# Kernel tuning notes

Measured on AMD Instinct MI355X. Metric: run time of the kernel, lower is better.

Reference implementation:

```python
import jax, jax.numpy as jnp
import numpy as np


def setup_inputs() -> dict:
    key = jax.random.key(0)
    k1, k2, k3 = jax.random.split(key, 3)
    B, S, I, H, M = 8, 2048, 256, 256, 1024
    x = jax.random.normal(k1, (B, S, I), dtype=jnp.float32)
    mem = jax.random.normal(k2, (B, M, H), dtype=jnp.float32)
    # Xavier-uniform with gain=sqrt(2): bound = sqrt(2)*sqrt(6/(H+I))
    bound = np.sqrt(2.0) * np.sqrt(6.0 / (H + I))
    W = jax.random.uniform(k3, (H, I), dtype=jnp.float32, minval=-bound, maxval=bound)
    return {"x": x, "mem": mem, "W": W}


def reference(x, mem, W):
    # key[b,s,h] = relu(sum_i x[b,s,i] * W[h,i])  -- one batched GEMM for all t
    key_seq = jax.nn.relu(jnp.einsum("bsi,hi->bsh", x, W))
    # val[b,s,m] = sum_h key[b,s,h] * mem[b,m,h]
    val_seq = jnp.einsum("bsh,bmh->bsm", key_seq, mem)
    return key_seq, val_seq
```

## Files before the change

kernel.cpp:

```cpp
#include <hip/hip_runtime.h>
#include <cstdint>

typedef unsigned short u16;
typedef __bf16 bf16x8 __attribute__((ext_vector_type(8)));
typedef float f32x4 __attribute__((ext_vector_type(4)));
typedef u16 u16x8 __attribute__((ext_vector_type(8)));

#define NX 4194304L
#define NW 65536L
#define NM 2097152L
#define WS_MEM (NW)
#define WS_KEY (NW + NM)

__device__ __forceinline__ u16 f2bf_rne(float f) {
  union { float f; uint32_t u; } v; v.f = f;
  uint32_t r = v.u + 0x7fffu + ((v.u >> 16) & 1u);
  return (u16)(r >> 16);
}

__global__ void convert_bf16_kernel(const float* __restrict__ mem,
                                    const float* __restrict__ W,
                                    u16* __restrict__ ws) {
  long e = ((long)blockIdx.x * blockDim.x + threadIdx.x) * 8;
  if (e >= NW + NM) return;
  const float* src; long l;
  if (e < NW) { src = W;   l = e; }
  else        { src = mem; l = e - NW; }
  float4 f0 = *(const float4*)(src + l);
  float4 f1 = *(const float4*)(src + l + 4);
  u16x8 o;
  o[0]=f2bf_rne(f0.x); o[1]=f2bf_rne(f0.y); o[2]=f2bf_rne(f0.z); o[3]=f2bf_rne(f0.w);
  o[4]=f2bf_rne(f1.x); o[5]=f2bf_rne(f1.y); o[6]=f2bf_rne(f1.z); o[7]=f2bf_rne(f1.w);
  *(u16x8*)(ws + e) = o;
}

#define BM 128
#define BN 128
#define BK 32

__device__ __forceinline__ u16x8 cvt8(float4 a, float4 b) {
  u16x8 o;
  o[0]=f2bf_rne(a.x); o[1]=f2bf_rne(a.y); o[2]=f2bf_rne(a.z); o[3]=f2bf_rne(a.w);
  o[4]=f2bf_rne(b.x); o[5]=f2bf_rne(b.y); o[6]=f2bf_rne(b.z); o[7]=f2bf_rne(b.w);
  return o;
}

template<bool CONVERT_A, bool RELU, bool STORE_BF16>
__global__ __launch_bounds__(256, 3)
void gemm_nt(const void* __restrict__ Ap, const u16* __restrict__ B,
             float* __restrict__ C, u16* __restrict__ Cbf,
             int M, int N, int K,
             long sA_batch, long sB_batch, long sC_batch)
{
  __shared__ __align__(16) u16 sA[2][BM * BK];
  __shared__ __align__(16) u16 sB[2][BN * BK];
  const int tid  = threadIdx.x;
  const int wave = tid >> 6;
  const int lane = tid & 63;
  const int quad = lane >> 4;
  const int r    = lane & 15;
  const int wm   = wave >> 1;
  const int wn   = wave & 1;

  const int gx  = gridDim.x, gy = gridDim.y;
  const int nwg = gx * gy * (int)gridDim.z;
  const int id  = (int)blockIdx.x + gx * ((int)blockIdx.y + gy * (int)blockIdx.z);
  const int cpx = nwg >> 3;
  const int lid = (id & 7) * cpx + (id >> 3);
  const int bx  = lid % gx;
  const int tq  = lid / gx;
  const int by  = tq % gy;
  const int bz  = tq / gy;

  const int bm   = by * BM;
  const int bn   = bx * BN;
  const int batch = bz;

  const float* Af = CONVERT_A ? ((const float*)Ap + (long)batch * sA_batch) : nullptr;
  const char*  Ab = CONVERT_A ? nullptr : (const char*)((const u16*)Ap + (long)batch * sA_batch);
  const char*  Bb = (const char*)(B + (long)batch * sB_batch);
  const long ldr = (long)K * 2;

  f32x4 acc[4][4];
  #pragma unroll
  for (int i = 0; i < 4; i++)
    #pragma unroll
    for (int j = 0; j < 4; j++)
      acc[i][j] = f32x4{0.f, 0.f, 0.f, 0.f};

  const int o0 = wave * 1024 + lane * 16;

  auto stageB = [&](int buf, int kt) {
    #pragma unroll
    for (int rr = 0; rr < 2; rr++) {
      const int o    = rr * 4096 + o0;
      const int row  = o >> 6;
      const int colb = o & 63;
      const char* g = Bb + (long)(bn + row) * ldr + (long)kt * 2 + colb;
      char* l = (char*)&sB[buf][0] + rr * 4096 + wave * 1024;
      __builtin_amdgcn_global_load_lds((const __attribute__((address_space(1))) void*)g,
                                       (__attribute__((address_space(3))) void*)l, 16, 0, 0);
    }
  };
  auto stageA_lds = [&](int buf, int kt) {
    #pragma unroll
    for (int rr = 0; rr < 2; rr++) {
      const int o    = rr * 4096 + o0;
      const int row  = o >> 6;
      const int colb = o & 63;
      const char* g = Ab + (long)(bm + row) * ldr + (long)kt * 2 + colb;
      char* l = (char*)&sA[buf][0] + rr * 4096 + wave * 1024;
      __builtin_amdgcn_global_load_lds((const __attribute__((address_space(1))) void*)g,
                                       (__attribute__((address_space(3))) void*)l, 16, 0, 0);
    }
  };

  float4 xa[4];
  const int arow = tid >> 1;
  const int ac0  = (tid & 1) * 16;
  auto loadA_f32 = [&](int kt) {
    const float* g = Af + (long)(bm + arow) * K + kt + ac0;
    #pragma unroll
    for (int c = 0; c < 4; c++) xa[c] = *(const float4*)(g + c * 4);
  };
  auto writeA_cvt = [&](int buf) {
    u16* d = &sA[buf][arow * BK + ac0];
    *(u16x8*)d       = cvt8(xa[0], xa[1]);
    *(u16x8*)(d + 8) = cvt8(xa[2], xa[3]);
  };

  if (CONVERT_A) { loadA_f32(0); writeA_cvt(0); }
  else           { stageA_lds(0, 0); }
  stageB(0, 0);
  __syncthreads();

  const int NT = K / BK;
  for (int t = 0; t < NT; ++t) {
    const int cur = t & 1, nxt = cur ^ 1;
    const bool pf = (t + 1 < NT);
    if (pf) {
      if (CONVERT_A) loadA_f32((t + 1) * BK);
      else           stageA_lds(nxt, (t + 1) * BK);
      stageB(nxt, (t + 1) * BK);
    }

    bf16x8 af[4], bfr[4];
    #pragma unroll
    for (int i = 0; i < 4; i++)
      af[i] = *(const bf16x8*)&sA[cur][(wm * 64 + i * 16 + r) * BK + quad * 8];
    #pragma unroll
    for (int j = 0; j < 4; j++)
      bfr[j] = *(const bf16x8*)&sB[cur][(wn * 64 + j * 16 + r) * BK + quad * 8];
    #pragma unroll
    for (int i = 0; i < 4; i++)
      #pragma unroll
      for (int j = 0; j < 4; j++)
        acc[i][j] = __builtin_amdgcn_mfma_f32_16x16x32_bf16(af[i], bfr[j], acc[i][j], 0, 0, 0);

    if (CONVERT_A && pf) writeA_cvt(nxt);
    __syncthreads();
  }

  float* Co = C + (long)batch * sC_batch;
  u16*   Bo = STORE_BF16 ? (Cbf + (long)batch * sC_batch) : nullptr;
  #pragma unroll
  for (int i = 0; i < 4; i++) {
    #pragma unroll
    for (int j = 0; j < 4; j++) {
      #pragma unroll
      for (int reg = 0; reg < 4; reg++) {
        const int row = bm + wm * 64 + i * 16 + quad * 4 + reg;
        const int col = bn + wn * 64 + j * 16 + r;
        float v = acc[i][j][reg];
        if (RELU) v = v > 0.f ? v : 0.f;
        const long idx = (long)row * N + col;
        Co[idx] = v;
        if (STORE_BF16) Bo[idx] = f2bf_rne(v);
      }
    }
  }
}

extern "C" void kernel_launch(void* const* d_in, const int* in_sizes, int n_in,
                              void* d_out, int out_size, void* d_ws, size_t ws_size,
                              hipStream_t stream) {
  const float* x   = (const float*)d_in[0];
  const float* mem = (const float*)d_in[1];
  const float* W   = (const float*)d_in[2];
  float* out   = (float*)d_out;
  float* key_f = out;
  float* val_f = out + NX;
  u16* ws     = (u16*)d_ws;
  u16* W_bf   = ws;
  u16* mem_bf = ws + WS_MEM;
  u16* key_bf = ws + WS_KEY;

  convert_bf16_kernel<<<(int)((NW + NM) / 8 / 256), 256, 0, stream>>>(mem, W, ws);

  dim3 g1(256 / BN, 16384 / BM, 1);
  gemm_nt<true, true, true><<<g1, 256, 0, stream>>>(x, W_bf, key_f, key_bf,
                                                    16384, 256, 256, 0, 0, 0);

  dim3 g2(1024 / BN, 2048 / BM, 8);
  gemm_nt<false, false, false><<<g2, 256, 0, stream>>>(key_bf, mem_bf, val_f, nullptr,
                                                       2048, 1024, 256,
                                                       (long)2048 * 256, (long)1024 * 256,
                                                       (long)2048 * 1024);
}
```

Before: 126.0 us.

## Fuse bf16 conversion into GEMM loads and drop separate convert kernel

Removes the standalone fp32-to-bf16 conversion kernel and the bf16 key copy. Both GEMMs now read fp32 operands directly and convert them in registers before writing to LDS. This saves one launch plus the workspace writes and reads. In exchange, B operands are read as fp32 (twice the bytes, re-read by many tiles), and the async global_load_lds path is replaced by register-staged loads with conversion ALU work.

```diff
diff --git a/kernel.cpp b/kernel.cpp
--- a/kernel.cpp
+++ b/kernel.cpp
@@ -7,36 +7,12 @@
 typedef u16 u16x8 __attribute__((ext_vector_type(8)));
 
 #define NX 4194304L
-#define NW 65536L
-#define NM 2097152L
-#define WS_MEM (NW)
-#define WS_KEY (NW + NM)
 
 __device__ __forceinline__ u16 f2bf_rne(float f) {
   union { float f; uint32_t u; } v; v.f = f;
   uint32_t r = v.u + 0x7fffu + ((v.u >> 16) & 1u);
   return (u16)(r >> 16);
 }
-
-__global__ void convert_bf16_kernel(const float* __restrict__ mem,
-                                    const float* __restrict__ W,
-                                    u16* __restrict__ ws) {
-  long e = ((long)blockIdx.x * blockDim.x + threadIdx.x) * 8;
-  if (e >= NW + NM) return;
-  const float* src; long l;
-  if (e < NW) { src = W;   l = e; }
-  else        { src = mem; l = e - NW; }
-  float4 f0 = *(const float4*)(src + l);
-  float4 f1 = *(const float4*)(src + l + 4);
-  u16x8 o;
-  o[0]=f2bf_rne(f0.x); o[1]=f2bf_rne(f0.y); o[2]=f2bf_rne(f0.z); o[3]=f2bf_rne(f0.w);
-  o[4]=f2bf_rne(f1.x); o[5]=f2bf_rne(f1.y); o[6]=f2bf_rne(f1.z); o[7]=f2bf_rne(f1.w);
-  *(u16x8*)(ws + e) = o;
-}
-
-#define BM 128
-#define BN 128
-#define BK 32
 
 __device__ __forceinline__ u16x8 cvt8(float4 a, float4 b) {
   u16x8 o;
@@ -45,12 +21,16 @@
   return o;
 }
 
-template<bool CONVERT_A, bool RELU, bool STORE_BF16>
+#define BM 128
+#define BN 128
+#define BK 32
+
+template<bool RELU>
 __global__ __launch_bounds__(256, 3)
-void gemm_nt(const void* __restrict__ Ap, const u16* __restrict__ B,
-             float* __restrict__ C, u16* __restrict__ Cbf,
-             int M, int N, int K,
-             long sA_batch, long sB_batch, long sC_batch)
+void gemm_nt_f32(const float* __restrict__ A, const float* __restrict__ B,
+                 float* __restrict__ C,
+                 int M, int N, int K,
+                 long sA_batch, long sB_batch, long sC_batch)
 {
   __shared__ __align__(16) u16 sA[2][BM * BK];
   __shared__ __align__(16) u16 sB[2][BN * BK];
@@ -72,14 +52,12 @@
   const int by  = tq % gy;
   const int bz  = tq / gy;
 
-  const int bm   = by * BM;
-  const int bn   = bx * BN;
+  const int bm    = by * BM;
+  const int bn    = bx * BN;
   const int batch = bz;
 
-  const float* Af = CONVERT_A ? ((const float*)Ap + (long)batch * sA_batch) : nullptr;
-  const char*  Ab = CONVERT_A ? nullptr : (const char*)((const u16*)Ap + (long)batch * sA_batch);
-  const char*  Bb = (const char*)(B + (long)batch * sB_batch);
-  const long ldr = (long)K * 2;
+  const float* Af = A + (long)batch * sA_batch;
+  const float* Bf = B + (long)batch * sB_batch;
 
   f32x4 acc[4][4];
   #pragma unroll
@@ -88,50 +66,33 @@
     for (int j = 0; j < 4; j++)
       acc[i][j] = f32x4{0.f, 0.f, 0.f, 0.f};
 
-  const int o0 = wave * 1024 + lane * 16;
-
-  auto stageB = [&](int buf, int kt) {
-    #pragma unroll
-    for (int rr = 0; rr < 2; rr++) {
-      const int o    = rr * 4096 + o0;
-      const int row  = o >> 6;
-      const int colb = o & 63;
-      const char* g = Bb + (long)(bn + row) * ldr + (long)kt * 2 + colb;
-      char* l = (char*)&sB[buf][0] + rr * 4096 + wave * 1024;
-      __builtin_amdgcn_global_load_lds((const __attribute__((address_space(1))) void*)g,
-                                       (__attribute__((address_space(3))) void*)l, 16, 0, 0);
-    }
-  };
-  auto stageA_lds = [&](int buf, int kt) {
-    #pragma unroll
-    for (int rr = 0; rr < 2; rr++) {
-      const int o    = rr * 4096 + o0;
-      const int row  = o >> 6;
-      const int colb = o & 63;
-      const char* g = Ab + (long)(bm + row) * ldr + (long)kt * 2 + colb;
-      char* l = (char*)&sA[buf][0] + rr * 4096 + wave * 1024;
-      __builtin_amdgcn_global_load_lds((const __attribute__((address_space(1))) void*)g,
-                                       (__attribute__((address_space(3))) void*)l, 16, 0, 0);
-    }
-  };
-
-  float4 xa[4];
+  float4 xa[4], xb[4];
   const int arow = tid >> 1;
   const int ac0  = (tid & 1) * 16;
-  auto loadA_f32 = [&](int kt) {
+
+  auto loadA = [&](int kt) {
     const float* g = Af + (long)(bm + arow) * K + kt + ac0;
     #pragma unroll
     for (int c = 0; c < 4; c++) xa[c] = *(const float4*)(g + c * 4);
   };
-  auto writeA_cvt = [&](int buf) {
+  auto loadB = [&](int kt) {
+    const float* g = Bf + (long)(bn + arow) * K + kt + ac0;
+    #pragma unroll
+    for (int c = 0; c < 4; c++) xb[c] = *(const float4*)(g + c * 4);
+  };
+  auto writeA = [&](int buf) {
     u16* d = &sA[buf][arow * BK + ac0];
     *(u16x8*)d       = cvt8(xa[0], xa[1]);
     *(u16x8*)(d + 8) = cvt8(xa[2], xa[3]);
   };
+  auto writeB = [&](int buf) {
+    u16* d = &sB[buf][arow * BK + ac0];
+    *(u16x8*)d       = cvt8(xb[0], xb[1]);
+    *(u16x8*)(d + 8) = cvt8(xb[2], xb[3]);
+  };
 
-  if (CONVERT_A) { loadA_f32(0); writeA_cvt(0); }
-  else           { stageA_lds(0, 0); }
-  stageB(0, 0);
+  loadA(0); loadB(0);
+  writeA(0); writeB(0);
   __syncthreads();
 
   const int NT = K / BK;
@@ -139,9 +100,8 @@
     const int cur = t & 1, nxt = cur ^ 1;
     const bool pf = (t + 1 < NT);
     if (pf) {
-      if (CONVERT_A) loadA_f32((t + 1) * BK);
-      else           stageA_lds(nxt, (t + 1) * BK);
-      stageB(nxt, (t + 1) * BK);
+      loadA((t + 1) * BK);
+      loadB((t + 1) * BK);
     }
 
     bf16x8 af[4], bfr[4];
@@ -157,12 +117,14 @@
       for (int j = 0; j < 4; j++)
         acc[i][j] = __builtin_amdgcn_mfma_f32_16x16x32_bf16(af[i], bfr[j], acc[i][j], 0, 0, 0);
 
-    if (CONVERT_A && pf) writeA_cvt(nxt);
+    if (pf) {
+      writeA(nxt);
+      writeB(nxt);
+    }
     __syncthreads();
   }
 
   float* Co = C + (long)batch * sC_batch;
-  u16*   Bo = STORE_BF16 ? (Cbf + (long)batch * sC_batch) : nullptr;
   #pragma unroll
   for (int i = 0; i < 4; i++) {
     #pragma unroll
@@ -173,9 +135,7 @@
         const int col = bn + wn * 64 + j * 16 + r;
         float v = acc[i][j][reg];
         if (RELU) v = v > 0.f ? v : 0.f;
-        const long idx = (long)row * N + col;
-        Co[idx] = v;
-        if (STORE_BF16) Bo[idx] = f2bf_rne(v);
+        Co[(long)row * N + col] = v;
       }
     }
   }
@@ -190,20 +150,15 @@
   float* out   = (float*)d_out;
   float* key_f = out;
   float* val_f = out + NX;
-  u16* ws     = (u16*)d_ws;
-  u16* W_bf   = ws;
-  u16* mem_bf = ws + WS_MEM;
-  u16* key_bf = ws + WS_KEY;
-
-  convert_bf16_kernel<<<(int)((NW + NM) / 8 / 256), 256, 0, stream>>>(mem, W, ws);
+  (void)d_ws; (void)ws_size;
 
   dim3 g1(256 / BN, 16384 / BM, 1);
-  gemm_nt<true, true, true><<<g1, 256, 0, stream>>>(x, W_bf, key_f, key_bf,
-                                                    16384, 256, 256, 0, 0, 0);
+  gemm_nt_f32<true><<<g1, 256, 0, stream>>>(x, W, key_f,
+                                            16384, 256, 256, 0, 0, 0);
 
   dim3 g2(1024 / BN, 2048 / BM, 8);
-  gemm_nt<false, false, false><<<g2, 256, 0, stream>>>(key_bf, mem_bf, val_f, nullptr,
-                                                       2048, 1024, 256,
-                                                       (long)2048 * 256, (long)1024 * 256,
-                                                       (long)2048 * 1024);
+  gemm_nt_f32<false><<<g2, 256, 0, stream>>>(key_f, mem, val_f,
+                                             2048, 1024, 256,
+                                             (long)2048 * 256, (long)1024 * 256,
+                                             (long)2048 * 1024);
 }
```

Measured after the change: 128.3 us. Within noise of the previous version (+1.9%).
